# Optimization experiments

Hardware: AMD Instinct MI355X
Metric: run time of the kernel (lower is better)

The kernel has to match this reference:

```python
import jax, jax.numpy as jnp
import numpy as np

B, Q, S, D, H = 8, 100, 4096, 256, 8
HD = D // H
EPS = 1e-5


def layer_norm(x, g, b):
    mu = jnp.mean(x, axis=-1, keepdims=True)
    var = jnp.mean(jnp.square(x - mu), axis=-1, keepdims=True)
    return (x - mu) * jax.lax.rsqrt(var + EPS) * g + b


def mha(q_in, k_in, v_in, w_in, b_in, w_out, b_out, bias=None):
    # torch nn.MultiheadAttention math (batch_first, dropout=0)
    wq, wk, wv = jnp.split(w_in, 3, axis=0)
    bq, bk, bv = jnp.split(b_in, 3, axis=0)
    Bq, Lq, _ = q_in.shape
    Lk = k_in.shape[1]
    q = (q_in @ wq.T + bq).reshape(Bq, Lq, H, HD)
    k = (k_in @ wk.T + bk).reshape(Bq, Lk, H, HD)
    v = (v_in @ wv.T + bv).reshape(Bq, Lk, H, HD)
    scores = jnp.einsum('bqhd,bkhd->bhqk', q, k) / jnp.sqrt(jnp.asarray(HD, q.dtype))
    if bias is not None:
        scores = scores + bias  # [B,1,Q,S] broadcast over heads (same per head)
    attn = jax.nn.softmax(scores, axis=-1)
    out = jnp.einsum('bhqk,bkhd->bqhd', attn, v).reshape(Bq, Lq, D)
    return out @ w_out.T + b_out


def setup_inputs() -> dict:
    key = jax.random.key(0)
    ks = jax.random.split(key, 12)
    s = 0.02
    return {
        'queries': jax.random.normal(ks[0], (B, Q, D), jnp.float32),
        'pixel_feat': jax.random.normal(ks[1], (B, S, D), jnp.float32),
        'prev_mask': jax.random.normal(ks[2], (B, Q, S), jnp.float32),
        'cross_in_w': jax.random.normal(ks[3], (3 * D, D), jnp.float32) * s,
        'cross_in_b': jnp.zeros((3 * D,), jnp.float32),
        'cross_out_w': jax.random.normal(ks[4], (D, D), jnp.float32) * s,
        'cross_out_b': jnp.zeros((D,), jnp.float32),
        'self_in_w': jax.random.normal(ks[5], (3 * D, D), jnp.float32) * s,
        'self_in_b': jnp.zeros((3 * D,), jnp.float32),
        'self_out_w': jax.random.normal(ks[6], (D, D), jnp.float32) * s,
        'self_out_b': jnp.zeros((D,), jnp.float32),
        'ln_cross_g': jnp.ones((D,), jnp.float32),
        'ln_cross_b': jnp.zeros((D,), jnp.float32),
        'ln_self_g': jnp.ones((D,), jnp.float32),
        'ln_self_b': jnp.zeros((D,), jnp.float32),
        'ln_ffn_g': jnp.ones((D,), jnp.float32),
        'ln_ffn_b': jnp.zeros((D,), jnp.float32),
        'ffn_w1': jax.random.normal(ks[7], (4 * D, D), jnp.float32) * s,
        'ffn_b1': jnp.zeros((4 * D,), jnp.float32),
        'ffn_w2': jax.random.normal(ks[8], (D, 4 * D), jnp.float32) * s,
        'ffn_b2': jnp.zeros((D,), jnp.float32),
    }


def reference(queries, pixel_feat, prev_mask,
              cross_in_w, cross_in_b, cross_out_w, cross_out_b,
              self_in_w, self_in_b, self_out_w, self_out_b,
              ln_cross_g, ln_cross_b, ln_self_g, ln_self_b, ln_ffn_g, ln_ffn_b,
              ffn_w1, ffn_b1, ffn_w2, ffn_b2):
    # masked cross-attn bias (no-grad region in torch; boolean ops have no grad)
    region = jax.nn.sigmoid(prev_mask) > 0.5                    # [B,Q,S]
    any_pos = jnp.any(region, axis=-1, keepdims=True)
    region = jnp.where(any_pos, region, jnp.ones_like(region))
    bias = (~region).astype(queries.dtype) * -10000.0
    bias = bias[:, None, :, :]                                  # [B,1,Q,S]

    q_out = mha(layer_norm(queries, ln_cross_g, ln_cross_b), pixel_feat, pixel_feat,
                cross_in_w, cross_in_b, cross_out_w, cross_out_b, bias)
    queries = queries + q_out

    q_norm = layer_norm(queries, ln_self_g, ln_self_b)
    q_out = mha(q_norm, q_norm, q_norm, self_in_w, self_in_b, self_out_w, self_out_b)
    queries = queries + q_out

    h = layer_norm(queries, ln_ffn_g, ln_ffn_b)
    h = jax.nn.gelu(h @ ffn_w1.T + ffn_b1, approximate=False) @ ffn_w2.T + ffn_b2
    return queries + h
```

## Files before the change

kernel.cpp:

```cpp
#include <hip/hip_runtime.h>
#include <hip/hip_bf16.h>
#include <math.h>

#define BQ 100
#define SB 8
#define SS 4096
#define DD 256
#define HH 8
#define HDD 32
#define NSPLIT 4
#define SCHUNK (SS / NSPLIT)
#define MROWS 800

typedef __attribute__((ext_vector_type(8))) short bf16x8;
typedef __attribute__((ext_vector_type(4))) float f32x4;

__device__ inline unsigned short f2bf(float f) {
    union { float f; unsigned u; } v; v.f = f;
    unsigned r = v.u + 0x7fff + ((v.u >> 16) & 1);
    return (unsigned short)(r >> 16);
}

__device__ inline unsigned pkbf(float x, float y) {
    union { __hip_bfloat162 h; unsigned u; } c;
// ... 190 lines not shown
        typedef unsigned short (*arow_t)[264];
        arow_t Aq = (arow_t)smem;
        float* mu_s = (float*)(smem + 16896);
        float* rs_s = mu_s + 32;
        float (*prt)[8][2] = (float(*)[8][2])(rs_s + 32);
        int idx = bid - 1824;
        int nq = idx & 1, my = idx >> 1;
        int m0 = my * 32;
        int row = t & 31, cs = t >> 5;
        const float* xp = queries + (size_t)(m0 + row) * DD + cs * 32;
        float s = 0.f, ss = 0.f;
#pragma unroll
        for (int c = 0; c < 32; c += 4) {
            float4 v = *(const float4*)(xp + c);
            s += v.x + v.y + v.z + v.w;
            ss += v.x * v.x + v.y * v.y + v.z * v.z + v.w * v.w;
        }
        prt[row][cs][0] = s; prt[row][cs][1] = ss;
        __syncthreads();
        if (t < 32) {
            float sum = 0.f, sq = 0.f;
#pragma unroll
            for (int k = 0; k < 8; k++) { sum += prt[t][k][0]; sq += prt[t][k][1]; }
            float mu = sum * (1.0f / DD);
            float var = sq * (1.0f / DD) - mu * mu;
            mu_s[t] = mu;
            rs_s[t] = rsqrtf(var + 1e-5f);
        }
        __syncthreads();
        {
            float mu = mu_s[row], r = rs_s[row];
            int col0 = cs * 32;
#pragma unroll
            for (int c = 0; c < 32; c += 8) {
                int col = col0 + c;
                float4 v0 = *(const float4*)(xp + c);
                float4 v1 = *(const float4*)(xp + c + 4);
                float4 g0 = *(const float4*)(ln_g + col);
                float4 g1 = *(const float4*)(ln_g + col + 4);
                float4 b0 = *(const float4*)(ln_b + col);
                float4 b1 = *(const float4*)(ln_b + col + 4);
                uint4 pk;
                pk.x = pkbf((v0.x - mu) * r * g0.x + b0.x, (v0.y - mu) * r * g0.y + b0.y);
                pk.y = pkbf((v0.z - mu) * r * g0.z + b0.z, (v0.w - mu) * r * g0.w + b0.w);
                pk.z = pkbf((v1.x - mu) * r * g1.x + b1.x, (v1.y - mu) * r * g1.y + b1.y);
                pk.w = pkbf((v1.z - mu) * r * g1.z + b1.z, (v1.w - mu) * r * g1.w + b1.w);
                *(uint4*)&Aq[row][col] = pk;
            }
        }
        __syncthreads();
        int w = t >> 6, lane = t & 63;
        int fr = lane & 15, quad = lane >> 4;
        int n0 = nq * 128 + w * 32;
        f32x4 acc[2][2] = {};
        const unsigned short* Wq0 = wbf + (size_t)(n0 + fr) * DD + quad * 8;
        const unsigned short* Wq1 = Wq0 + (size_t)16 * DD;
#pragma unroll
        for (int k0 = 0; k0 < DD; k0 += 32) {
            bf16x8 a0 = *(const bf16x8*)&Aq[fr][k0 + quad * 8];
            bf16x8 a1 = *(const bf16x8*)&Aq[16 + fr][k0 + quad * 8];
            bf16x8 w0 = *(const bf16x8*)(Wq0 + k0);
            bf16x8 w1 = *(const bf16x8*)(Wq1 + k0);
            acc[0][0] = __builtin_amdgcn_mfma_f32_16x16x32_bf16(a0, w0, acc[0][0], 0, 0, 0);
            acc[0][1] = __builtin_amdgcn_mfma_f32_16x16x32_bf16(a0, w1, acc[0][1], 0, 0, 0);
            acc[1][0] = __builtin_amdgcn_mfma_f32_16x16x32_bf16(a1, w0, acc[1][0], 0, 0, 0);
            acc[1][1] = __builtin_amdgcn_mfma_f32_16x16x32_bf16(a1, w1, acc[1][1], 0, 0, 0);
        }
#pragma unroll
        for (int ni = 0; ni < 2; ni++) {
            int n = n0 + ni * 16 + fr;
            float bv = cb[n];
#pragma unroll
            for (int mi = 0; mi < 2; mi++) {
#pragma unroll
                for (int r = 0; r < 4; r++) {
                    int m = m0 + mi * 16 + quad * 4 + r;
                    q_cross[(size_t)m * DD + n] = acc[mi][ni][r] + bv;
                }
            }
        }
    }
}

template<int MODE>
__global__ __launch_bounds__(64, 4) void ln_gemm(
        const float* __restrict__ X, const float* __restrict__ gam,
        const float* __restrict__ bet,
        const unsigned short* __restrict__ W, const float* __restrict__ bias,
        const float* __restrict__ res,
        float* __restrict__ C, int N) {
    __shared__ unsigned short As[32][264];
    __shared__ float mu_s[32], rs_s[32];
    __shared__ float prt[32][2][2];
    const int t = threadIdx.x;
    const int fr = t & 15, quad = t >> 4;
    const int m0 = blockIdx.y * 32, n0 = blockIdx.x * 32;
    const int row = t & 31, half = t >> 5;

    const float* xp = X + (size_t)(m0 + row) * DD + half * 128;
    float s = 0.f, ss = 0.f;
#pragma unroll
    for (int c = 0; c < 128; c += 4) {
        float4 v = *(const float4*)(xp + c);
        s += v.x + v.y + v.z + v.w;
        ss += v.x * v.x + v.y * v.y + v.z * v.z + v.w * v.w;
    }
    prt[row][half][0] = s;
    prt[row][half][1] = ss;
    __syncthreads();
    if (t < 32) {
        float sum = prt[t][0][0] + prt[t][1][0];
        float sq  = prt[t][0][1] + prt[t][1][1];
        float mu = sum * (1.0f / DD);
        float var = sq * (1.0f / DD) - mu * mu;
        mu_s[t] = mu;
        rs_s[t] = rsqrtf(var + 1e-5f);
    }
    __syncthreads();
    {
        float mu = mu_s[row], r = rs_s[row];
#pragma unroll
        for (int c = 0; c < 128; c += 8) {
            int col = half * 128 + c;
            float4 v0 = *(const float4*)(xp + c);
            float4 v1 = *(const float4*)(xp + c + 4);
            float4 g0 = *(const float4*)(gam + col);
            float4 g1 = *(const float4*)(gam + col + 4);
            float4 b0 = *(const float4*)(bet + col);
            float4 b1 = *(const float4*)(bet + col + 4);
            uint4 pk;
            pk.x = pkbf((v0.x - mu) * r * g0.x + b0.x, (v0.y - mu) * r * g0.y + b0.y);
            pk.y = pkbf((v0.z - mu) * r * g0.z + b0.z, (v0.w - mu) * r * g0.w + b0.w);
            pk.z = pkbf((v1.x - mu) * r * g1.x + b1.x, (v1.y - mu) * r * g1.y + b1.y);
            pk.w = pkbf((v1.z - mu) * r * g1.z + b1.z, (v1.w - mu) * r * g1.w + b1.w);
            *(uint4*)&As[row][col] = pk;
        }
    }
    __syncthreads();

    f32x4 acc[2][2] = {};
    const unsigned short* Wp0 = W + (size_t)(n0 + fr) * DD + quad * 8;
    const unsigned short* Wp1 = Wp0 + (size_t)16 * DD;
#pragma unroll
    for (int k0 = 0; k0 < DD; k0 += 32) {
        bf16x8 a0 = *(const bf16x8*)&As[fr][k0 + quad * 8];
        bf16x8 a1 = *(const bf16x8*)&As[16 + fr][k0 + quad * 8];
        bf16x8 w0 = *(const bf16x8*)(Wp0 + k0);
        bf16x8 w1 = *(const bf16x8*)(Wp1 + k0);
        acc[0][0] = __builtin_amdgcn_mfma_f32_16x16x32_bf16(a0, w0, acc[0][0], 0, 0, 0);
        acc[0][1] = __builtin_amdgcn_mfma_f32_16x16x32_bf16(a0, w1, acc[0][1], 0, 0, 0);
        acc[1][0] = __builtin_amdgcn_mfma_f32_16x16x32_bf16(a1, w0, acc[1][0], 0, 0, 0);
        acc[1][1] = __builtin_amdgcn_mfma_f32_16x16x32_bf16(a1, w1, acc[1][1], 0, 0, 0);
    }

#pragma unroll
    for (int ni = 0; ni < 2; ni++) {
        int n = n0 + ni * 16 + fr;
        float bv = bias[n];
#pragma unroll
        for (int mi = 0; mi < 2; mi++) {
#pragma unroll
            for (int r = 0; r < 4; r++) {
                int m = m0 + mi * 16 + quad * 4 + r;
                float v = acc[mi][ni][r] + bv;
                if (MODE == 1) {
                    v = 0.5f * v * (1.0f + erff(v * 0.70710678118654752f));
                } else if (MODE == 2) {
                    v += res[(size_t)m * N + n];
                }
                C[(size_t)m * N + n] = v;
            }
        }
    }
}

__global__ __launch_bounds__(64, 4) void comb_gemm(
        const float* __restrict__ Opart, const float* __restrict__ mpart,
        const float* __restrict__ lpart,
        const unsigned short* __restrict__ W, const float* __restrict__ bias,
        const float* __restrict__ res,
        float* __restrict__ C) {
    __shared__ unsigned short As[32][264];
    const int t = threadIdx.x;
    const int fr = t & 15, quad = t >> 4;
    const int m0 = blockIdx.y * 32, n0 = blockIdx.x * 32;
    const int row = t & 31, half = t >> 5;

    {
        int m = m0 + row;
        int b = m / BQ, q = m % BQ;
#pragma unroll
        for (int h = half * 4; h < half * 4 + 4; h++) {
            float mv[NSPLIT], wsp[NSPLIT];
            float mstar = -1e30f;
#pragma unroll
            for (int sp = 0; sp < NSPLIT; sp++) {
                mv[sp] = mpart[((size_t)(b * NSPLIT + sp) * HH + h) * BQ + q];
                mstar = fmaxf(mstar, mv[sp]);
            }
            float lstar = 0.f;
#pragma unroll
            for (int sp = 0; sp < NSPLIT; sp++) {
                wsp[sp] = __expf(mv[sp] - mstar);
                lstar += lpart[((size_t)(b * NSPLIT + sp) * HH + h) * BQ + q] * wsp[sp];
            }
            float inv = 1.0f / lstar;
#pragma unroll
            for (int d = 0; d < HDD; d += 8) {
                float o[8] = {};
#pragma unroll
                for (int sp = 0; sp < NSPLIT; sp++) {
                    const float* op = Opart +
                        ((size_t)(b * NSPLIT + sp) * BQ + q) * DD + h * HDD + d;
                    float4 a = *(const float4*)op;
                    float4 b4 = *(const float4*)(op + 4);
                    o[0] += a.x * wsp[sp];  o[1] += a.y * wsp[sp];
                    o[2] += a.z * wsp[sp];  o[3] += a.w * wsp[sp];
                    o[4] += b4.x * wsp[sp]; o[5] += b4.y * wsp[sp];
                    o[6] += b4.z * wsp[sp]; o[7] += b4.w * wsp[sp];
                }
                uint4 pk;
                pk.x = pkbf(o[0] * inv, o[1] * inv);
                pk.y = pkbf(o[2] * inv, o[3] * inv);
                pk.z = pkbf(o[4] * inv, o[5] * inv);
                pk.w = pkbf(o[6] * inv, o[7] * inv);
                *(uint4*)&As[row][h * HDD + d] = pk;
            }
        }
    }
    __syncthreads();

    f32x4 acc[2][2] = {};
    const unsigned short* Wp0 = W + (size_t)(n0 + fr) * DD + quad * 8;
    const unsigned short* Wp1 = Wp0 + (size_t)16 * DD;
#pragma unroll
    for (int k0 = 0; k0 < DD; k0 += 32) {
        bf16x8 a0 = *(const bf16x8*)&As[fr][k0 + quad * 8];
        bf16x8 a1 = *(const bf16x8*)&As[16 + fr][k0 + quad * 8];
        bf16x8 w0 = *(const bf16x8*)(Wp0 + k0);
        bf16x8 w1 = *(const bf16x8*)(Wp1 + k0);
        acc[0][0] = __builtin_amdgcn_mfma_f32_16x16x32_bf16(a0, w0, acc[0][0], 0, 0, 0);
        acc[0][1] = __builtin_amdgcn_mfma_f32_16x16x32_bf16(a0, w1, acc[0][1], 0, 0, 0);
        acc[1][0] = __builtin_amdgcn_mfma_f32_16x16x32_bf16(a1, w0, acc[1][0], 0, 0, 0);
        acc[1][1] = __builtin_amdgcn_mfma_f32_16x16x32_bf16(a1, w1, acc[1][1], 0, 0, 0);
    }

#pragma unroll
    for (int ni = 0; ni < 2; ni++) {
        int n = n0 + ni * 16 + fr;
        float bv = bias[n];
#pragma unroll
        for (int mi = 0; mi < 2; mi++) {
#pragma unroll
            for (int r = 0; r < 4; r++) {
                int m = m0 + mi * 16 + quad * 4 + r;
                float v = acc[mi][ni][r] + bv + res[(size_t)m * DD + n];
                C[(size_t)m * DD + n] = v;
            }
        }
    }
}

template<int KK, int SPLITK, int MODE>
__global__ __launch_bounds__(64, 4) void gemm_skinny2(
        const float* __restrict__ A, const unsigned short* __restrict__ W,
        const float* __restrict__ bias, const float* __restrict__ res,
        float* __restrict__ C, float* __restrict__ Cp, int N) {
    const int lane = threadIdx.x;
    const int fr = lane & 15, quad = lane >> 4;
    const int m0 = blockIdx.y * 32;
    const int n0 = blockIdx.x * 32;
    const int sk = blockIdx.z;
    const int KCH = KK / SPLITK;

    f32x4 acc[2][2] = {};
    const float* Ap0 = A + (size_t)(m0 + fr) * KK + sk * KCH + quad * 8;
    const float* Ap1 = Ap0 + (size_t)16 * KK;
    const unsigned short* Wp0 = W + (size_t)(n0 + fr) * KK + sk * KCH + quad * 8;
    const unsigned short* Wp1 = Wp0 + (size_t)16 * KK;

#pragma unroll
    for (int k0 = 0; k0 < KCH; k0 += 32) {
        bf16x8 a0 = load_bf8(Ap0 + k0);
        bf16x8 a1 = load_bf8(Ap1 + k0);
        bf16x8 w0 = *(const bf16x8*)(Wp0 + k0);
        bf16x8 w1 = *(const bf16x8*)(Wp1 + k0);
        acc[0][0] = __builtin_amdgcn_mfma_f32_16x16x32_bf16(a0, w0, acc[0][0], 0, 0, 0);
        acc[0][1] = __builtin_amdgcn_mfma_f32_16x16x32_bf16(a0, w1, acc[0][1], 0, 0, 0);
        acc[1][0] = __builtin_amdgcn_mfma_f32_16x16x32_bf16(a1, w0, acc[1][0], 0, 0, 0);
        acc[1][1] = __builtin_amdgcn_mfma_f32_16x16x32_bf16(a1, w1, acc[1][1], 0, 0, 0);
    }

    if (SPLITK == 1) {
#pragma unroll
        for (int ni = 0; ni < 2; ni++) {
            int n = n0 + ni * 16 + fr;
            float bv = bias[n];
#pragma unroll
            for (int mi = 0; mi < 2; mi++) {
#pragma unroll
                for (int r = 0; r < 4; r++) {
                    int m = m0 + mi * 16 + quad * 4 + r;
                    float v = acc[mi][ni][r] + bv;
                    if (MODE == 1) {
                        v = 0.5f * v * (1.0f + erff(v * 0.70710678118654752f));
                    } else if (MODE == 2) {
                        v += res[(size_t)m * N + n];
                    }
                    C[(size_t)m * N + n] = v;
                }
            }
        }
    } else {
        float* dst = Cp + (size_t)sk * MROWS * N;
#pragma unroll
        for (int ni = 0; ni < 2; ni++) {
            int n = n0 + ni * 16 + fr;
#pragma unroll
            for (int mi = 0; mi < 2; mi++) {
#pragma unroll
                for (int r = 0; r < 4; r++) {
                    int m = m0 + mi * 16 + quad * 4 + r;
                    dst[(size_t)m * N + n] = acc[mi][ni][r];
                }
            }
        }
    }
}

template<int SPLITK, int MODE>
__global__ void gemm_combine(const float* __restrict__ Cp,
                             const float* __restrict__ bias,
                             const float* __restrict__ res,
                             float* __restrict__ C, int N) {
    int m = blockIdx.x;
    for (int n = threadIdx.x; n < N; n += 256) {
        float v = bias[n];
#pragma unroll
        for (int sk = 0; sk < SPLITK; sk++)
            v += Cp[((size_t)sk * MROWS + m) * N + n];
        if (MODE == 1) {
            v = 0.5f * v * (1.0f + erff(v * 0.70710678118654752f));
        } else if (MODE == 2) {
            v += res[(size_t)m * N + n];
        }
        C[(size_t)m * N + n] = v;
    }
}

#define QT 64
#define ST 128

__global__ __launch_bounds__(256) void cross_attn_mfma(
        const float* __restrict__ Qm,
        const unsigned short* __restrict__ Kb,
        const unsigned short* __restrict__ Vb,
        const unsigned* __restrict__ Mbits,
        float* __restrict__ Opart,
        float* __restrict__ mpart,
        float* __restrict__ lpart) {
    __shared__ unsigned short Qs[QT][40];
    __shared__ unsigned short Ks[ST][40];
    __shared__ unsigned short Vt[HDD][136];
    __shared__ unsigned short Ps[QT][136];
    __shared__ unsigned Mq[QT][4];
    __shared__ float4 redm[QT];
    __shared__ float4 reds[QT];
    __shared__ float m_s[QT], alpha_s[QT], l_s[QT];

    const int qb = blockIdx.x, h = blockIdx.y;
    const int b = blockIdx.z / NSPLIT, sp = blockIdx.z % NSPLIT;
    const int t = threadIdx.x;
    const int w = t >> 6, lane = t & 63;
    const int fr = lane & 15, quad = lane >> 4;
    const int q0 = qb * QT;
    const int qlim = min(BQ - q0, QT);

    {
        int q = t >> 2, c0 = (t & 3) * 8;
        float4 v0 = make_float4(0.f, 0.f, 0.f, 0.f), v1 = v0;
        if (q < qlim) {
            const float* qp = Qm + (size_t)(b * BQ + q0 + q) * DD + h * HDD + c0;
            v0 = *(const float4*)qp;
            v1 = *(const float4*)(qp + 4);
        }
        const float sc = 0.17677669529663687f;
        uint4 pq;
        pq.x = pkbf(v0.x * sc, v0.y * sc);
        pq.y = pkbf(v0.z * sc, v0.w * sc);
        pq.z = pkbf(v1.x * sc, v1.y * sc);
        pq.w = pkbf(v1.z * sc, v1.w * sc);
        *(uint4*)&Qs[q][c0] = pq;
        if (t < QT) { m_s[t] = -1e30f; l_s[t] = 0.f; }
    }

    f32x4 oacc[2] = {};
    const unsigned short* Kbase = Kb + (((size_t)(b * HH + h)) * SS << 5);
    const unsigned short* Vbase = Vb + (((size_t)(b * HH + h)) << 5) * SS;

    for (int s0 = sp * SCHUNK; s0 < (sp + 1) * SCHUNK; s0 += ST) {
        __syncthreads();
        {
            int r = t >> 1, half = t & 1;
            const unsigned short* kp = Kbase + ((size_t)(s0 + r) << 5) + half * 16;
            *(uint4*)&Ks[r][half * 16] = *(const uint4*)kp;
            *(uint4*)&Ks[r][half * 16 + 8] = *(const uint4*)(kp + 8);
            int d = t >> 3, c = (t & 7) * 16;
            const unsigned short* vp = Vbase + (size_t)d * SS + s0 + c;
            *(uint4*)&Vt[d][c] = *(const uint4*)vp;
            *(uint4*)&Vt[d][c + 8] = *(const uint4*)(vp + 8);
        }
        {
            int q = t >> 2, wd = t & 3;
            unsigned mword = 0xFFFFFFFFu;
            if (q < qlim)
                mword = Mbits[(size_t)(b * BQ + q0 + q) * 128 + (s0 >> 5) + wd];
            Mq[q][wd] = mword;
        }
        __syncthreads();

        bf16x8 af[2];
#pragma unroll
        for (int mt = 0; mt < 2; mt++)
            af[mt] = *(const bf16x8*)&Ks[w * 32 + mt * 16 + fr][quad * 8];
        f32x4 st[2][4];
#pragma unroll
        for (int nt = 0; nt < 4; nt++) {
            bf16x8 bq = *(const bf16x8*)&Qs[nt * 16 + fr][quad * 8];
#pragma unroll
            for (int mt = 0; mt < 2; mt++) {
                f32x4 z = {0.f, 0.f, 0.f, 0.f};
                st[mt][nt] = __builtin_amdgcn_mfma_f32_16x16x32_bf16(af[mt], bq, z, 0, 0, 0);
// ... 181 lines not shown
    float pmax[7];
#pragma unroll
    for (int nt = 0; nt < 7; nt++) {
        pmax[nt] = -1e30f;
#pragma unroll
        for (int mt = 0; mt < 2; mt++)
#pragma unroll
            for (int r = 0; r < 4; r++) {
                int s = w * 32 + mt * 16 + quad * 4 + r;
                float v = st[mt][nt][r];
                if (s >= BQ) v = -1e30f;
                st[mt][nt][r] = v;
                pmax[nt] = fmaxf(pmax[nt], v);
            }
        red[nt * 16 + fr][w * 4 + quad] = pmax[nt];
    }
    __syncthreads();
    if (t < 112) {
        float m = -1e30f;
#pragma unroll
        for (int k = 0; k < 16; k++) m = fmaxf(m, red[t][k]);
        m_s[t] = m;
    }
    __syncthreads();

    float psum[7];
#pragma unroll
    for (int nt = 0; nt < 7; nt++) {
        float mrow = m_s[nt * 16 + fr];
        psum[nt] = 0.f;
#pragma unroll
        for (int mt = 0; mt < 2; mt++) {
            float p0 = __expf(st[mt][nt][0] - mrow);
            float p1 = __expf(st[mt][nt][1] - mrow);
            float p2 = __expf(st[mt][nt][2] - mrow);
            float p3 = __expf(st[mt][nt][3] - mrow);
            psum[nt] += p0 + p1 + p2 + p3;
            uint2 pk;
            pk.x = pkbf(p0, p1);
            pk.y = pkbf(p2, p3);
            *(uint2*)&Ps[nt * 16 + fr][w * 32 + mt * 16 + quad * 4] = pk;
        }
        red[nt * 16 + fr][w * 4 + quad] = psum[nt];
    }
    __syncthreads();
    if (t < 112) {
        float s = 0.f;
#pragma unroll
        for (int k = 0; k < 16; k++) s += red[t][k];
        l_s[t] = s;
    }
    __syncthreads();

    f32x4 oacc[2][2] = {};
#pragma unroll
    for (int ti = 0; ti < 2; ti++) {
        int qt = w + ti * 4;
        if (qt < 7) {
#pragma unroll
            for (int k0 = 0; k0 < 128; k0 += 32) {
                bf16x8 ap = *(const bf16x8*)&Ps[qt * 16 + fr][k0 + quad * 8];
                bf16x8 bv0 = *(const bf16x8*)&Vt[fr][k0 + quad * 8];
                bf16x8 bv1 = *(const bf16x8*)&Vt[16 + fr][k0 + quad * 8];
                oacc[ti][0] = __builtin_amdgcn_mfma_f32_16x16x32_bf16(ap, bv0, oacc[ti][0], 0, 0, 0);
                oacc[ti][1] = __builtin_amdgcn_mfma_f32_16x16x32_bf16(ap, bv1, oacc[ti][1], 0, 0, 0);
            }
        }
    }
#pragma unroll
    for (int ti = 0; ti < 2; ti++) {
        int qt = w + ti * 4;
        if (qt < 7) {
#pragma unroll
            for (int nd = 0; nd < 2; nd++) {
#pragma unroll
                for (int r = 0; r < 4; r++) {
                    int q = qt * 16 + quad * 4 + r;
                    if (q < BQ) {
                        float inv = 1.0f / l_s[q];
                        Out[(size_t)(b * BQ + q) * DD + h * HDD + nd * 16 + fr] =
                            oacc[ti][nd][r] * inv;
                    }
                }
            }
        }
    }
}

extern "C" void kernel_launch(void* const* d_in, const int* in_sizes, int n_in,
                              void* d_out, int out_size, void* d_ws, size_t ws_size,
                              hipStream_t stream) {
    const float* queries    = (const float*)d_in[0];
    const float* pixel_feat = (const float*)d_in[1];
    const float* prev_mask  = (const float*)d_in[2];
    const float* cross_in_w  = (const float*)d_in[3];
    const float* cross_in_b  = (const float*)d_in[4];
    const float* cross_out_w = (const float*)d_in[5];
    const float* cross_out_b = (const float*)d_in[6];
    const float* self_in_w   = (const float*)d_in[7];
    const float* self_in_b   = (const float*)d_in[8];
    const float* self_out_w  = (const float*)d_in[9];
    const float* self_out_b  = (const float*)d_in[10];
    const float* ln_cross_g  = (const float*)d_in[11];
    const float* ln_cross_b  = (const float*)d_in[12];
    const float* ln_self_g   = (const float*)d_in[13];
    const float* ln_self_b   = (const float*)d_in[14];
    const float* ln_ffn_g    = (const float*)d_in[15];
    const float* ln_ffn_b    = (const float*)d_in[16];
    const float* ffn_w1 = (const float*)d_in[17];
    const float* ffn_b1 = (const float*)d_in[18];
    const float* ffn_w2 = (const float*)d_in[19];
    const float* ffn_b2 = (const float*)d_in[20];
    float* out = (float*)d_out;

    const int NQ = SB * BQ;
    const int NK = SB * SS;

    float* ws = (float*)d_ws;
    unsigned* Mbits = (unsigned*)ws;   ws += (size_t)NQ * 128;
    float* q_cross  = ws;              ws += (size_t)NQ * DD;
    unsigned short* Kbk = (unsigned short*)ws;
    ws += (size_t)NK * DD / 2;
    unsigned short* Vbk = (unsigned short*)ws;
    ws += (size_t)NK * DD / 2;
    float* queries1 = ws;              ws += (size_t)NQ * DD;
    float* qkv      = ws;              ws += (size_t)NQ * 3 * DD;
    float* attn2    = ws;              ws += (size_t)NQ * DD;
    float* queries2 = ws;              ws += (size_t)NQ * DD;
    float* ffn_h    = ws;              ws += (size_t)NQ * 4 * DD;
    float* Csplit   = ws;              ws += (size_t)4 * MROWS * DD;
    float* Opart    = ws;              ws += (size_t)SB * NSPLIT * BQ * DD;
    float* mpart    = ws;              ws += (size_t)SB * NSPLIT * HH * BQ;
    float* lpart    = ws;              ws += (size_t)SB * NSPLIT * HH * BQ;
    unsigned short* wbf = (unsigned short*)ws;
    ws += WTOT / 2;
    unsigned short* Abf = (unsigned short*)ws;

    wprep<<<4608, 256, 0, stream>>>(
        cross_in_w, self_in_w, cross_out_w, self_out_w, ffn_w1, ffn_w2,
        pixel_feat, wbf, Abf);

    stage1<<<1874, 256, 0, stream>>>(
        queries, ln_cross_g, ln_cross_b, wbf, cross_in_b, q_cross,
        Abf, Kbk, Vbk, prev_mask, Mbits);

    cross_attn_mfma<<<dim3(2, HH, SB * NSPLIT), 256, 0, stream>>>(
        q_cross, Kbk, Vbk, Mbits, Opart, mpart, lpart);
    comb_gemm<<<dim3(8, 25), 64, 0, stream>>>(
        Opart, mpart, lpart, wbf + WOFF_COW, cross_out_b, queries, queries1);

    ln_gemm<0><<<dim3(24, 25), 64, 0, stream>>>(
        queries1, ln_self_g, ln_self_b, wbf + WOFF_SIW, self_in_b, nullptr,
        qkv, 3 * DD);
    self_attn_mfma<<<dim3(HH, SB), 256, 0, stream>>>(qkv, attn2);
    gemm_skinny2<256, 1, 2><<<dim3(8, 25), 64, 0, stream>>>(
        attn2, wbf + WOFF_SOW, self_out_b, queries1, queries2, nullptr, DD);

    ln_gemm<1><<<dim3(32, 25), 64, 0, stream>>>(
        queries2, ln_ffn_g, ln_ffn_b, wbf + WOFF_F1, ffn_b1, nullptr,
        ffn_h, 4 * DD);
    gemm_skinny2<1024, 4, 2><<<dim3(8, 25, 4), 64, 0, stream>>>(
        ffn_h, wbf + WOFF_F2, ffn_b2, nullptr, nullptr, Csplit, DD);
    gemm_combine<4, 2><<<MROWS, 256, 0, stream>>>(
        Csplit, ffn_b2, queries2, out, DD);
}
```

Measured before the change: 231.0 us.

## Fuse post-attention GEMM chain into three row-block kernels

Replaces the small per-tile GEMM launches (comb_gemm, ln_gemm, gemm_skinny2, gemm_combine) with three fused kernels. Each kernel handles a 32-row block across the full width: attention combine plus out-projection plus LayerNorm plus QKV, then self out-projection plus LayerNorm plus FFN1 with GELU, then FFN2 plus residual. The FFN hidden activation is stored as bf16 and the split-K reduction is removed. This cuts launch count and intermediate global traffic, but each kernel now runs only 25 blocks, so the GPU is far less parallel.

```diff
diff --git a/kernel.cpp b/kernel.cpp
--- a/kernel.cpp
+++ b/kernel.cpp
@@ -296,272 +296,6 @@
     }
 }
 
-template<int MODE>
-__global__ __launch_bounds__(64, 4) void ln_gemm(
-        const float* __restrict__ X, const float* __restrict__ gam,
-        const float* __restrict__ bet,
-        const unsigned short* __restrict__ W, const float* __restrict__ bias,
-        const float* __restrict__ res,
-        float* __restrict__ C, int N) {
-    __shared__ unsigned short As[32][264];
-    __shared__ float mu_s[32], rs_s[32];
-    __shared__ float prt[32][2][2];
-    const int t = threadIdx.x;
-    const int fr = t & 15, quad = t >> 4;
-    const int m0 = blockIdx.y * 32, n0 = blockIdx.x * 32;
-    const int row = t & 31, half = t >> 5;
-
-    const float* xp = X + (size_t)(m0 + row) * DD + half * 128;
-    float s = 0.f, ss = 0.f;
-#pragma unroll
-    for (int c = 0; c < 128; c += 4) {
-        float4 v = *(const float4*)(xp + c);
-        s += v.x + v.y + v.z + v.w;
-        ss += v.x * v.x + v.y * v.y + v.z * v.z + v.w * v.w;
-    }
-    prt[row][half][0] = s;
-    prt[row][half][1] = ss;
-    __syncthreads();
-    if (t < 32) {
-        float sum = prt[t][0][0] + prt[t][1][0];
-        float sq  = prt[t][0][1] + prt[t][1][1];
-        float mu = sum * (1.0f / DD);
-        float var = sq * (1.0f / DD) - mu * mu;
-        mu_s[t] = mu;
-        rs_s[t] = rsqrtf(var + 1e-5f);
-    }
-    __syncthreads();
-    {
-        float mu = mu_s[row], r = rs_s[row];
-#pragma unroll
-        for (int c = 0; c < 128; c += 8) {
-            int col = half * 128 + c;
-            float4 v0 = *(const float4*)(xp + c);
-            float4 v1 = *(const float4*)(xp + c + 4);
-            float4 g0 = *(const float4*)(gam + col);
-            float4 g1 = *(const float4*)(gam + col + 4);
-            float4 b0 = *(const float4*)(bet + col);
-            float4 b1 = *(const float4*)(bet + col + 4);
-            uint4 pk;
-            pk.x = pkbf((v0.x - mu) * r * g0.x + b0.x, (v0.y - mu) * r * g0.y + b0.y);
-            pk.y = pkbf((v0.z - mu) * r * g0.z + b0.z, (v0.w - mu) * r * g0.w + b0.w);
-            pk.z = pkbf((v1.x - mu) * r * g1.x + b1.x, (v1.y - mu) * r * g1.y + b1.y);
-            pk.w = pkbf((v1.z - mu) * r * g1.z + b1.z, (v1.w - mu) * r * g1.w + b1.w);
-            *(uint4*)&As[row][col] = pk;
-        }
-    }
-    __syncthreads();
-
-    f32x4 acc[2][2] = {};
-    const unsigned short* Wp0 = W + (size_t)(n0 + fr) * DD + quad * 8;
-    const unsigned short* Wp1 = Wp0 + (size_t)16 * DD;
-#pragma unroll
-    for (int k0 = 0; k0 < DD; k0 += 32) {
-        bf16x8 a0 = *(const bf16x8*)&As[fr][k0 + quad * 8];
-        bf16x8 a1 = *(const bf16x8*)&As[16 + fr][k0 + quad * 8];
-        bf16x8 w0 = *(const bf16x8*)(Wp0 + k0);
-        bf16x8 w1 = *(const bf16x8*)(Wp1 + k0);
-        acc[0][0] = __builtin_amdgcn_mfma_f32_16x16x32_bf16(a0, w0, acc[0][0], 0, 0, 0);
-        acc[0][1] = __builtin_amdgcn_mfma_f32_16x16x32_bf16(a0, w1, acc[0][1], 0, 0, 0);
-        acc[1][0] = __builtin_amdgcn_mfma_f32_16x16x32_bf16(a1, w0, acc[1][0], 0, 0, 0);
-        acc[1][1] = __builtin_amdgcn_mfma_f32_16x16x32_bf16(a1, w1, acc[1][1], 0, 0, 0);
-    }
-
-#pragma unroll
-    for (int ni = 0; ni < 2; ni++) {
-        int n = n0 + ni * 16 + fr;
-        float bv = bias[n];
-#pragma unroll
-        for (int mi = 0; mi < 2; mi++) {
-#pragma unroll
-            for (int r = 0; r < 4; r++) {
-                int m = m0 + mi * 16 + quad * 4 + r;
-                float v = acc[mi][ni][r] + bv;
-                if (MODE == 1) {
-                    v = 0.5f * v * (1.0f + erff(v * 0.70710678118654752f));
-                } else if (MODE == 2) {
-                    v += res[(size_t)m * N + n];
-                }
-                C[(size_t)m * N + n] = v;
-            }
-        }
-    }
-}
-
-__global__ __launch_bounds__(64, 4) void comb_gemm(
-        const float* __restrict__ Opart, const float* __restrict__ mpart,
-        const float* __restrict__ lpart,
-        const unsigned short* __restrict__ W, const float* __restrict__ bias,
-        const float* __restrict__ res,
-        float* __restrict__ C) {
-    __shared__ unsigned short As[32][264];
-    const int t = threadIdx.x;
-    const int fr = t & 15, quad = t >> 4;
-    const int m0 = blockIdx.y * 32, n0 = blockIdx.x * 32;
-    const int row = t & 31, half = t >> 5;
-
-    {
-        int m = m0 + row;
-        int b = m / BQ, q = m % BQ;
-#pragma unroll
-        for (int h = half * 4; h < half * 4 + 4; h++) {
-            float mv[NSPLIT], wsp[NSPLIT];
-            float mstar = -1e30f;
-#pragma unroll
-            for (int sp = 0; sp < NSPLIT; sp++) {
-                mv[sp] = mpart[((size_t)(b * NSPLIT + sp) * HH + h) * BQ + q];
-                mstar = fmaxf(mstar, mv[sp]);
-            }
-            float lstar = 0.f;
-#pragma unroll
-            for (int sp = 0; sp < NSPLIT; sp++) {
-                wsp[sp] = __expf(mv[sp] - mstar);
-                lstar += lpart[((size_t)(b * NSPLIT + sp) * HH + h) * BQ + q] * wsp[sp];
-            }
-            float inv = 1.0f / lstar;
-#pragma unroll
-            for (int d = 0; d < HDD; d += 8) {
-                float o[8] = {};
-#pragma unroll
-                for (int sp = 0; sp < NSPLIT; sp++) {
-                    const float* op = Opart +
-                        ((size_t)(b * NSPLIT + sp) * BQ + q) * DD + h * HDD + d;
-                    float4 a = *(const float4*)op;
-                    float4 b4 = *(const float4*)(op + 4);
-                    o[0] += a.x * wsp[sp];  o[1] += a.y * wsp[sp];
-                    o[2] += a.z * wsp[sp];  o[3] += a.w * wsp[sp];
-                    o[4] += b4.x * wsp[sp]; o[5] += b4.y * wsp[sp];
-                    o[6] += b4.z * wsp[sp]; o[7] += b4.w * wsp[sp];
-                }
-                uint4 pk;
-                pk.x = pkbf(o[0] * inv, o[1] * inv);
-                pk.y = pkbf(o[2] * inv, o[3] * inv);
-                pk.z = pkbf(o[4] * inv, o[5] * inv);
-                pk.w = pkbf(o[6] * inv, o[7] * inv);
-                *(uint4*)&As[row][h * HDD + d] = pk;
-            }
-        }
-    }
-    __syncthreads();
-
-    f32x4 acc[2][2] = {};
-    const unsigned short* Wp0 = W + (size_t)(n0 + fr) * DD + quad * 8;
-    const unsigned short* Wp1 = Wp0 + (size_t)16 * DD;
-#pragma unroll
-    for (int k0 = 0; k0 < DD; k0 += 32) {
-        bf16x8 a0 = *(const bf16x8*)&As[fr][k0 + quad * 8];
-        bf16x8 a1 = *(const bf16x8*)&As[16 + fr][k0 + quad * 8];
-        bf16x8 w0 = *(const bf16x8*)(Wp0 + k0);
-        bf16x8 w1 = *(const bf16x8*)(Wp1 + k0);
-        acc[0][0] = __builtin_amdgcn_mfma_f32_16x16x32_bf16(a0, w0, acc[0][0], 0, 0, 0);
-        acc[0][1] = __builtin_amdgcn_mfma_f32_16x16x32_bf16(a0, w1, acc[0][1], 0, 0, 0);
-        acc[1][0] = __builtin_amdgcn_mfma_f32_16x16x32_bf16(a1, w0, acc[1][0], 0, 0, 0);
-        acc[1][1] = __builtin_amdgcn_mfma_f32_16x16x32_bf16(a1, w1, acc[1][1], 0, 0, 0);
-    }
-
-#pragma unroll
-    for (int ni = 0; ni < 2; ni++) {
-        int n = n0 + ni * 16 + fr;
-        float bv = bias[n];
-#pragma unroll
-        for (int mi = 0; mi < 2; mi++) {
-#pragma unroll
-            for (int r = 0; r < 4; r++) {
-                int m = m0 + mi * 16 + quad * 4 + r;
-                float v = acc[mi][ni][r] + bv + res[(size_t)m * DD + n];
-                C[(size_t)m * DD + n] = v;
-            }
-        }
-    }
-}
-
-template<int KK, int SPLITK, int MODE>
-__global__ __launch_bounds__(64, 4) void gemm_skinny2(
-        const float* __restrict__ A, const unsigned short* __restrict__ W,
-        const float* __restrict__ bias, const float* __restrict__ res,
-        float* __restrict__ C, float* __restrict__ Cp, int N) {
-    const int lane = threadIdx.x;
-    const int fr = lane & 15, quad = lane >> 4;
-    const int m0 = blockIdx.y * 32;
-    const int n0 = blockIdx.x * 32;
-    const int sk = blockIdx.z;
-    const int KCH = KK / SPLITK;
-
-    f32x4 acc[2][2] = {};
-    const float* Ap0 = A + (size_t)(m0 + fr) * KK + sk * KCH + quad * 8;
-    const float* Ap1 = Ap0 + (size_t)16 * KK;
-    const unsigned short* Wp0 = W + (size_t)(n0 + fr) * KK + sk * KCH + quad * 8;
-    const unsigned short* Wp1 = Wp0 + (size_t)16 * KK;
-
-#pragma unroll
-    for (int k0 = 0; k0 < KCH; k0 += 32) {
-        bf16x8 a0 = load_bf8(Ap0 + k0);
-        bf16x8 a1 = load_bf8(Ap1 + k0);
-        bf16x8 w0 = *(const bf16x8*)(Wp0 + k0);
-        bf16x8 w1 = *(const bf16x8*)(Wp1 + k0);
-        acc[0][0] = __builtin_amdgcn_mfma_f32_16x16x32_bf16(a0, w0, acc[0][0], 0, 0, 0);
-        acc[0][1] = __builtin_amdgcn_mfma_f32_16x16x32_bf16(a0, w1, acc[0][1], 0, 0, 0);
-        acc[1][0] = __builtin_amdgcn_mfma_f32_16x16x32_bf16(a1, w0, acc[1][0], 0, 0, 0);
-        acc[1][1] = __builtin_amdgcn_mfma_f32_16x16x32_bf16(a1, w1, acc[1][1], 0, 0, 0);
-    }
-
-    if (SPLITK == 1) {
-#pragma unroll
-        for (int ni = 0; ni < 2; ni++) {
-            int n = n0 + ni * 16 + fr;
-            float bv = bias[n];
-#pragma unroll
-            for (int mi = 0; mi < 2; mi++) {
-#pragma unroll
-                for (int r = 0; r < 4; r++) {
-                    int m = m0 + mi * 16 + quad * 4 + r;
-                    float v = acc[mi][ni][r] + bv;
-                    if (MODE == 1) {
-                        v = 0.5f * v * (1.0f + erff(v * 0.70710678118654752f));
-                    } else if (MODE == 2) {
-                        v += res[(size_t)m * N + n];
-                    }
-                    C[(size_t)m * N + n] = v;
-                }
-            }
-        }
-    } else {
-        float* dst = Cp + (size_t)sk * MROWS * N;
-#pragma unroll
-        for (int ni = 0; ni < 2; ni++) {
-            int n = n0 + ni * 16 + fr;
-#pragma unroll
-            for (int mi = 0; mi < 2; mi++) {
-#pragma unroll
-                for (int r = 0; r < 4; r++) {
-                    int m = m0 + mi * 16 + quad * 4 + r;
-                    dst[(size_t)m * N + n] = acc[mi][ni][r];
-                }
-            }
-        }
-    }
-}
-
-template<int SPLITK, int MODE>
-__global__ void gemm_combine(const float* __restrict__ Cp,
-                             const float* __restrict__ bias,
-                             const float* __restrict__ res,
-                             float* __restrict__ C, int N) {
-    int m = blockIdx.x;
-    for (int n = threadIdx.x; n < N; n += 256) {
-        float v = bias[n];
-#pragma unroll
-        for (int sk = 0; sk < SPLITK; sk++)
-            v += Cp[((size_t)sk * MROWS + m) * N + n];
-        if (MODE == 1) {
-            v = 0.5f * v * (1.0f + erff(v * 0.70710678118654752f));
-        } else if (MODE == 2) {
-            v += res[(size_t)m * N + n];
-        }
-        C[(size_t)m * N + n] = v;
-    }
-}
-
 #define QT 64
 #define ST 128
 
@@ -909,6 +643,345 @@
                             oacc[ti][nd][r] * inv;
                     }
                 }
+            }
+        }
+    }
+}
+
+__global__ __launch_bounds__(256) void fused_comb_qkv(
+        const float* __restrict__ Opart, const float* __restrict__ mpart,
+        const float* __restrict__ lpart,
+        const unsigned short* __restrict__ Wout, const float* __restrict__ bout,
+        const float* __restrict__ resid,
+        const float* __restrict__ gam, const float* __restrict__ bet,
+        const unsigned short* __restrict__ Wqkv, const float* __restrict__ bqkv,
+        float* __restrict__ queries1, float* __restrict__ qkv) {
+    __shared__ unsigned short As[32][264];
+    __shared__ float V32[32][264];
+    __shared__ float prt[32][8][2];
+    __shared__ float mu_s[32], rs_s[32];
+    const int t = threadIdx.x;
+    const int m0 = blockIdx.x * 32;
+    const int w = t >> 6, lane = t & 63;
+    const int fr = lane & 15, quad = lane >> 4;
+
+    {
+        int row = t & 31, h = t >> 5;
+        int m = m0 + row;
+        int b = m / BQ, q = m % BQ;
+        float mv[NSPLIT], wsp[NSPLIT];
+        float mstar = -1e30f;
+#pragma unroll
+        for (int sp = 0; sp < NSPLIT; sp++) {
+            mv[sp] = mpart[((size_t)(b * NSPLIT + sp) * HH + h) * BQ + q];
+            mstar = fmaxf(mstar, mv[sp]);
+        }
+        float lstar = 0.f;
+#pragma unroll
+        for (int sp = 0; sp < NSPLIT; sp++) {
+            wsp[sp] = __expf(mv[sp] - mstar);
+            lstar += lpart[((size_t)(b * NSPLIT + sp) * HH + h) * BQ + q] * wsp[sp];
+        }
+        float inv = 1.0f / lstar;
+#pragma unroll
+        for (int d = 0; d < HDD; d += 8) {
+            float o[8] = {};
+#pragma unroll
+            for (int sp = 0; sp < NSPLIT; sp++) {
+                const float* op = Opart +
+                    ((size_t)(b * NSPLIT + sp) * BQ + q) * DD + h * HDD + d;
+                float4 a = *(const float4*)op;
+                float4 b4 = *(const float4*)(op + 4);
+                o[0] += a.x * wsp[sp];  o[1] += a.y * wsp[sp];
+                o[2] += a.z * wsp[sp];  o[3] += a.w * wsp[sp];
+                o[4] += b4.x * wsp[sp]; o[5] += b4.y * wsp[sp];
+                o[6] += b4.z * wsp[sp]; o[7] += b4.w * wsp[sp];
+            }
+            uint4 pk;
+            pk.x = pkbf(o[0] * inv, o[1] * inv);
+            pk.y = pkbf(o[2] * inv, o[3] * inv);
+            pk.z = pkbf(o[4] * inv, o[5] * inv);
+            pk.w = pkbf(o[6] * inv, o[7] * inv);
+            *(uint4*)&As[row][h * HDD + d] = pk;
+        }
+    }
+    __syncthreads();
+
+    {
+        f32x4 acc[2][4] = {};
+        const unsigned short* Wp = Wout + (size_t)(w * 64 + fr) * DD + quad * 8;
+#pragma unroll
+        for (int k0 = 0; k0 < DD; k0 += 32) {
+            bf16x8 a0 = *(const bf16x8*)&As[fr][k0 + quad * 8];
+            bf16x8 a1 = *(const bf16x8*)&As[16 + fr][k0 + quad * 8];
+#pragma unroll
+            for (int ni = 0; ni < 4; ni++) {
+                bf16x8 wv = *(const bf16x8*)(Wp + (size_t)ni * 16 * DD + k0);
+                acc[0][ni] = __builtin_amdgcn_mfma_f32_16x16x32_bf16(a0, wv, acc[0][ni], 0, 0, 0);
+                acc[1][ni] = __builtin_amdgcn_mfma_f32_16x16x32_bf16(a1, wv, acc[1][ni], 0, 0, 0);
+            }
+        }
+#pragma unroll
+        for (int ni = 0; ni < 4; ni++) {
+            int n = w * 64 + ni * 16 + fr;
+            float bv = bout[n];
+#pragma unroll
+            for (int mi = 0; mi < 2; mi++) {
+#pragma unroll
+                for (int r = 0; r < 4; r++) {
+                    int row = mi * 16 + quad * 4 + r;
+                    float v = acc[mi][ni][r] + bv + resid[(size_t)(m0 + row) * DD + n];
+                    V32[row][n] = v;
+                    queries1[(size_t)(m0 + row) * DD + n] = v;
+                }
+            }
+        }
+    }
+    __syncthreads();
+
+    {
+        int row = t & 31, cs = t >> 5;
+        float s = 0.f, ss = 0.f;
+#pragma unroll
+        for (int c = 0; c < 32; c += 4) {
+            float4 v = *(const float4*)&V32[row][cs * 32 + c];
+            s += v.x + v.y + v.z + v.w;
+            ss += v.x * v.x + v.y * v.y + v.z * v.z + v.w * v.w;
+        }
+        prt[row][cs][0] = s; prt[row][cs][1] = ss;
+        __syncthreads();
+        if (t < 32) {
+            float sum = 0.f, sq = 0.f;
+#pragma unroll
+            for (int k = 0; k < 8; k++) { sum += prt[t][k][0]; sq += prt[t][k][1]; }
+            float mu = sum * (1.0f / DD);
+            float var = sq * (1.0f / DD) - mu * mu;
+            mu_s[t] = mu;
+            rs_s[t] = rsqrtf(var + 1e-5f);
+        }
+        __syncthreads();
+        float mu = mu_s[row], rr = rs_s[row];
+#pragma unroll
+        for (int c = 0; c < 32; c += 8) {
+            int col = cs * 32 + c;
+            float4 v0 = *(const float4*)&V32[row][col];
+            float4 v1 = *(const float4*)&V32[row][col + 4];
+            float4 g0 = *(const float4*)(gam + col);
+            float4 g1 = *(const float4*)(gam + col + 4);
+            float4 b0 = *(const float4*)(bet + col);
+            float4 b1 = *(const float4*)(bet + col + 4);
+            uint4 pk;
+            pk.x = pkbf((v0.x - mu) * rr * g0.x + b0.x, (v0.y - mu) * rr * g0.y + b0.y);
+            pk.y = pkbf((v0.z - mu) * rr * g0.z + b0.z, (v0.w - mu) * rr * g0.w + b0.w);
+            pk.z = pkbf((v1.x - mu) * rr * g1.x + b1.x, (v1.y - mu) * rr * g1.y + b1.y);
+            pk.w = pkbf((v1.z - mu) * rr * g1.z + b1.z, (v1.w - mu) * rr * g1.w + b1.w);
+            *(uint4*)&As[row][col] = pk;
+        }
+    }
+    __syncthreads();
+
+#pragma unroll
+    for (int p = 0; p < 3; p++) {
+        f32x4 acc[2][4] = {};
+        const unsigned short* Wp = Wqkv + (size_t)(p * 256 + w * 64 + fr) * DD + quad * 8;
+#pragma unroll
+        for (int k0 = 0; k0 < DD; k0 += 32) {
+            bf16x8 a0 = *(const bf16x8*)&As[fr][k0 + quad * 8];
+            bf16x8 a1 = *(const bf16x8*)&As[16 + fr][k0 + quad * 8];
+#pragma unroll
+            for (int ni = 0; ni < 4; ni++) {
+                bf16x8 wv = *(const bf16x8*)(Wp + (size_t)ni * 16 * DD + k0);
+                acc[0][ni] = __builtin_amdgcn_mfma_f32_16x16x32_bf16(a0, wv, acc[0][ni], 0, 0, 0);
+                acc[1][ni] = __builtin_amdgcn_mfma_f32_16x16x32_bf16(a1, wv, acc[1][ni], 0, 0, 0);
+            }
+        }
+#pragma unroll
+        for (int ni = 0; ni < 4; ni++) {
+            int n = p * 256 + w * 64 + ni * 16 + fr;
+            float bv = bqkv[n];
+#pragma unroll
+            for (int mi = 0; mi < 2; mi++) {
+#pragma unroll
+                for (int r = 0; r < 4; r++) {
+                    int m = m0 + mi * 16 + quad * 4 + r;
+                    qkv[(size_t)m * 768 + n] = acc[mi][ni][r] + bv;
+                }
+            }
+        }
+    }
+}
+
+__global__ __launch_bounds__(256) void fused_proj_ffn1(
+        const float* __restrict__ attn2,
+        const unsigned short* __restrict__ Wout, const float* __restrict__ bout,
+        const float* __restrict__ resid,
+        const float* __restrict__ gam, const float* __restrict__ bet,
+        const unsigned short* __restrict__ W1, const float* __restrict__ b1,
+        float* __restrict__ queries2, unsigned short* __restrict__ Hbf) {
+    __shared__ unsigned short As[32][264];
+    __shared__ float V32[32][264];
+    __shared__ float prt[32][8][2];
+    __shared__ float mu_s[32], rs_s[32];
+    const int t = threadIdx.x;
+    const int m0 = blockIdx.x * 32;
+    const int w = t >> 6, lane = t & 63;
+    const int fr = lane & 15, quad = lane >> 4;
+
+    {
+        int row = t & 31, cs = t >> 5;
+        const float* xp = attn2 + (size_t)(m0 + row) * DD + cs * 32;
+#pragma unroll
+        for (int c = 0; c < 32; c += 8) {
+            float4 v0 = *(const float4*)(xp + c);
+            float4 v1 = *(const float4*)(xp + c + 4);
+            uint4 pk;
+            pk.x = pkbf(v0.x, v0.y); pk.y = pkbf(v0.z, v0.w);
+            pk.z = pkbf(v1.x, v1.y); pk.w = pkbf(v1.z, v1.w);
+            *(uint4*)&As[row][cs * 32 + c] = pk;
+        }
+    }
+    __syncthreads();
+
+    {
+        f32x4 acc[2][4] = {};
+        const unsigned short* Wp = Wout + (size_t)(w * 64 + fr) * DD + quad * 8;
+#pragma unroll
+        for (int k0 = 0; k0 < DD; k0 += 32) {
+            bf16x8 a0 = *(const bf16x8*)&As[fr][k0 + quad * 8];
+            bf16x8 a1 = *(const bf16x8*)&As[16 + fr][k0 + quad * 8];
+#pragma unroll
+            for (int ni = 0; ni < 4; ni++) {
+                bf16x8 wv = *(const bf16x8*)(Wp + (size_t)ni * 16 * DD + k0);
+                acc[0][ni] = __builtin_amdgcn_mfma_f32_16x16x32_bf16(a0, wv, acc[0][ni], 0, 0, 0);
+                acc[1][ni] = __builtin_amdgcn_mfma_f32_16x16x32_bf16(a1, wv, acc[1][ni], 0, 0, 0);
+            }
+        }
+#pragma unroll
+        for (int ni = 0; ni < 4; ni++) {
+            int n = w * 64 + ni * 16 + fr;
+            float bv = bout[n];
+#pragma unroll
+            for (int mi = 0; mi < 2; mi++) {
+#pragma unroll
+                for (int r = 0; r < 4; r++) {
+                    int row = mi * 16 + quad * 4 + r;
+                    float v = acc[mi][ni][r] + bv + resid[(size_t)(m0 + row) * DD + n];
+                    V32[row][n] = v;
+                    queries2[(size_t)(m0 + row) * DD + n] = v;
+                }
+            }
+        }
+    }
+    __syncthreads();
+
+    {
+        int row = t & 31, cs = t >> 5;
+        float s = 0.f, ss = 0.f;
+#pragma unroll
+        for (int c = 0; c < 32; c += 4) {
+            float4 v = *(const float4*)&V32[row][cs * 32 + c];
+            s += v.x + v.y + v.z + v.w;
+            ss += v.x * v.x + v.y * v.y + v.z * v.z + v.w * v.w;
+        }
+        prt[row][cs][0] = s; prt[row][cs][1] = ss;
+        __syncthreads();
+        if (t < 32) {
+            float sum = 0.f, sq = 0.f;
+#pragma unroll
+            for (int k = 0; k < 8; k++) { sum += prt[t][k][0]; sq += prt[t][k][1]; }
+            float mu = sum * (1.0f / DD);
+            float var = sq * (1.0f / DD) - mu * mu;
+            mu_s[t] = mu;
+            rs_s[t] = rsqrtf(var + 1e-5f);
+        }
+        __syncthreads();
+        float mu = mu_s[row], rr = rs_s[row];
+#pragma unroll
+        for (int c = 0; c < 32; c += 8) {
+            int col = cs * 32 + c;
+            float4 v0 = *(const float4*)&V32[row][col];
+            float4 v1 = *(const float4*)&V32[row][col + 4];
+            float4 g0 = *(const float4*)(gam + col);
+            float4 g1 = *(const float4*)(gam + col + 4);
+            float4 b0 = *(const float4*)(bet + col);
+            float4 b1 = *(const float4*)(bet + col + 4);
+            uint4 pk;
+            pk.x = pkbf((v0.x - mu) * rr * g0.x + b0.x, (v0.y - mu) * rr * g0.y + b0.y);
+            pk.y = pkbf((v0.z - mu) * rr * g0.z + b0.z, (v0.w - mu) * rr * g0.w + b0.w);
+            pk.z = pkbf((v1.x - mu) * rr * g1.x + b1.x, (v1.y - mu) * rr * g1.y + b1.y);
+            pk.w = pkbf((v1.z - mu) * rr * g1.z + b1.z, (v1.w - mu) * rr * g1.w + b1.w);
+            *(uint4*)&As[row][col] = pk;
+        }
+    }
+    __syncthreads();
+
+#pragma unroll
+    for (int p = 0; p < 4; p++) {
+        f32x4 acc[2][4] = {};
+        const unsigned short* Wp = W1 + (size_t)(p * 256 + w * 64 + fr) * DD + quad * 8;
+#pragma unroll
+        for (int k0 = 0; k0 < DD; k0 += 32) {
+            bf16x8 a0 = *(const bf16x8*)&As[fr][k0 + quad * 8];
+            bf16x8 a1 = *(const bf16x8*)&As[16 + fr][k0 + quad * 8];
+#pragma unroll
+            for (int ni = 0; ni < 4; ni++) {
+                bf16x8 wv = *(const bf16x8*)(Wp + (size_t)ni * 16 * DD + k0);
+                acc[0][ni] = __builtin_amdgcn_mfma_f32_16x16x32_bf16(a0, wv, acc[0][ni], 0, 0, 0);
+                acc[1][ni] = __builtin_amdgcn_mfma_f32_16x16x32_bf16(a1, wv, acc[1][ni], 0, 0, 0);
+            }
+        }
+#pragma unroll
+        for (int ni = 0; ni < 4; ni++) {
+            int n = p * 256 + w * 64 + ni * 16 + fr;
+            float bv = b1[n];
+#pragma unroll
+            for (int mi = 0; mi < 2; mi++) {
+#pragma unroll
+                for (int r = 0; r < 4; r++) {
+                    int m = m0 + mi * 16 + quad * 4 + r;
+                    float v = acc[mi][ni][r] + bv;
+                    v = 0.5f * v * (1.0f + erff(v * 0.70710678118654752f));
+                    Hbf[(size_t)m * 1024 + n] = f2bf(v);
+                }
+            }
+        }
+    }
+}
+
+__global__ __launch_bounds__(256) void fused_ffn2(
+        const unsigned short* __restrict__ Hbf,
+        const unsigned short* __restrict__ W2, const float* __restrict__ b2,
+        const float* __restrict__ resid, float* __restrict__ out) {
+    const int t = threadIdx.x;
+    const int m0 = blockIdx.x * 32;
+    const int w = t >> 6, lane = t & 63;
+    const int fr = lane & 15, quad = lane >> 4;
+
+    f32x4 acc[2][4] = {};
+    const unsigned short* Ap0 = Hbf + (size_t)(m0 + fr) * 1024 + quad * 8;
+    const unsigned short* Ap1 = Ap0 + (size_t)16 * 1024;
+    const unsigned short* Wp = W2 + (size_t)(w * 64 + fr) * 1024 + quad * 8;
+#pragma unroll 4
+    for (int k0 = 0; k0 < 1024; k0 += 32) {
+        bf16x8 a0 = *(const bf16x8*)(Ap0 + k0);
+        bf16x8 a1 = *(const bf16x8*)(Ap1 + k0);
+#pragma unroll
+        for (int ni = 0; ni < 4; ni++) {
+            bf16x8 wv = *(const bf16x8*)(Wp + (size_t)ni * 16 * 1024 + k0);
+            acc[0][ni] = __builtin_amdgcn_mfma_f32_16x16x32_bf16(a0, wv, acc[0][ni], 0, 0, 0);
+            acc[1][ni] = __builtin_amdgcn_mfma_f32_16x16x32_bf16(a1, wv, acc[1][ni], 0, 0, 0);
+        }
+    }
+#pragma unroll
+    for (int ni = 0; ni < 4; ni++) {
+        int n = w * 64 + ni * 16 + fr;
+        float bv = b2[n];
+#pragma unroll
+        for (int mi = 0; mi < 2; mi++) {
+#pragma unroll
+            for (int r = 0; r < 4; r++) {
+                int m = m0 + mi * 16 + quad * 4 + r;
+                out[(size_t)m * DD + n] = acc[mi][ni][r] + bv + resid[(size_t)m * DD + n];
             }
         }
     }
@@ -955,13 +1028,13 @@
     float* attn2    = ws;              ws += (size_t)NQ * DD;
     float* queries2 = ws;              ws += (size_t)NQ * DD;
     float* ffn_h    = ws;              ws += (size_t)NQ * 4 * DD;
-    float* Csplit   = ws;              ws += (size_t)4 * MROWS * DD;
     float* Opart    = ws;              ws += (size_t)SB * NSPLIT * BQ * DD;
     float* mpart    = ws;              ws += (size_t)SB * NSPLIT * HH * BQ;
     float* lpart    = ws;              ws += (size_t)SB * NSPLIT * HH * BQ;
     unsigned short* wbf = (unsigned short*)ws;
     ws += WTOT / 2;
     unsigned short* Abf = (unsigned short*)ws;
+    unsigned short* Hbf = (unsigned short*)ffn_h;
 
     wprep<<<4608, 256, 0, stream>>>(
         cross_in_w, self_in_w, cross_out_w, self_out_w, ffn_w1, ffn_w2,
@@ -973,21 +1046,14 @@
 
     cross_attn_mfma<<<dim3(2, HH, SB * NSPLIT), 256, 0, stream>>>(
         q_cross, Kbk, Vbk, Mbits, Opart, mpart, lpart);
-    comb_gemm<<<dim3(8, 25), 64, 0, stream>>>(
-        Opart, mpart, lpart, wbf + WOFF_COW, cross_out_b, queries, queries1);
-
-    ln_gemm<0><<<dim3(24, 25), 64, 0, stream>>>(
-        queries1, ln_self_g, ln_self_b, wbf + WOFF_SIW, self_in_b, nullptr,
-        qkv, 3 * DD);
+
+    fused_comb_qkv<<<25, 256, 0, stream>>>(
+        Opart, mpart, lpart, wbf + WOFF_COW, cross_out_b, queries,
+        ln_self_g, ln_self_b, wbf + WOFF_SIW, self_in_b, queries1, qkv);
     self_attn_mfma<<<dim3(HH, SB), 256, 0, stream>>>(qkv, attn2);
-    gemm_skinny2<256, 1, 2><<<dim3(8, 25), 64, 0, stream>>>(
-        attn2, wbf + WOFF_SOW, self_out_b, queries1, queries2, nullptr, DD);
-
-    ln_gemm<1><<<dim3(32, 25), 64, 0, stream>>>(
-        queries2, ln_ffn_g, ln_ffn_b, wbf + WOFF_F1, ffn_b1, nullptr,
-        ffn_h, 4 * DD);
-    gemm_skinny2<1024, 4, 2><<<dim3(8, 25, 4), 64, 0, stream>>>(
-        ffn_h, wbf + WOFF_F2, ffn_b2, nullptr, nullptr, Csplit, DD);
-    gemm_combine<4, 2><<<MROWS, 256, 0, stream>>>(
-        Csplit, ffn_b2, queries2, out, DD);
-}
+    fused_proj_ffn1<<<25, 256, 0, stream>>>(
+        attn2, wbf + WOFF_SOW, self_out_b, queries1,
+        ln_ffn_g, ln_ffn_b, wbf + WOFF_F1, ffn_b1, queries2, Hbf);
+    fused_ffn2<<<25, 256, 0, stream>>>(
+        Hbf, wbf + WOFF_F2, ffn_b2, queries2, out);
+}
```

Measured after the change: 288.3 us. 24.8% more time.
